# Optimization experiments

Hardware: AMD Instinct MI355X
Metric: run time of the kernel (lower is better)

Reference implementation:

```python
import jax, jax.numpy as jnp
import numpy as np

B, S, C = 32, 1024, 12      # sentences, words per sentence, chars per word
E, H = 256, 512             # embedding dim, word-LSTM hidden dim
V, CS, T = 50000, 128, 50   # vocab, charset, tagset


def _lstm(x, Wih, Whh, b):
    """Standard torch LSTM (gate order i,f,g,o). x: [T, N, I] -> hidden trace [T, N, H]."""
    Hd = Whh.shape[1]
    N = x.shape[1]
    h0 = jnp.zeros((N, Hd), x.dtype)
    c0 = jnp.zeros((N, Hd), x.dtype)

    def step(carry, xt):
        h, c = carry
        gates = xt @ Wih.T + h @ Whh.T + b
        i, f, g, o = jnp.split(gates, 4, axis=-1)
        c = jax.nn.sigmoid(f) * c + jax.nn.sigmoid(i) * jnp.tanh(g)
        h = jax.nn.sigmoid(o) * jnp.tanh(c)
        return (h, c), h

    _, hs = jax.lax.scan(step, (h0, c0), x)
    return hs


def setup_inputs() -> dict:
    key = jax.random.key(0)
    ks = jax.random.split(key, 12)
    sc = 0.05
    return {
        "char_idx": jax.random.randint(ks[0], (B, S, C), 0, CS),
        "word_idx": jax.random.randint(ks[1], (B, S), 0, V),
        "char_emb": jax.random.normal(ks[2], (CS, E), jnp.float32) * sc,
        "word_emb": jax.random.normal(ks[3], (V, E), jnp.float32) * sc,
        "Wc_ih": jax.random.normal(ks[4], (4 * E, E), jnp.float32) * sc,
        "Wc_hh": jax.random.normal(ks[5], (4 * E, E), jnp.float32) * sc,
        "bc": jnp.zeros((4 * E,), jnp.float32),
        "Ww_ih": jax.random.normal(ks[6], (4 * H, 2 * E), jnp.float32) * sc,
        "Ww_hh": jax.random.normal(ks[7], (4 * H, H), jnp.float32) * sc,
        "bw": jnp.zeros((4 * H,), jnp.float32),
        "Wt": jax.random.normal(ks[8], (T, H), jnp.float32) * sc,
        "bt": jnp.zeros((T,), jnp.float32),
    }


def reference(char_idx, word_idx, char_emb, word_emb, Wc_ih, Wc_hh, bc,
              Ww_ih, Ww_hh, bw, Wt, bt):
    # --- character-level LSTM: each word starts from a fresh zero state ---
    ce = char_emb[char_idx]                       # [B, S, C, E]
    ce = ce.reshape(B * S, C, E).transpose(1, 0, 2)  # [C, B*S, E]
    char_hs = _lstm(ce, Wc_ih, Wc_hh, bc)         # [C, B*S, E]
    char_feat = char_hs[-1].reshape(B, S, E)      # last char output per word

    # --- word-level LSTM over concatenated [word_emb ; char_feat] ---
    we = word_emb[word_idx]                       # [B, S, E]
    x = jnp.concatenate([we, char_feat], axis=-1) # [B, S, 2E]
    x = x.transpose(1, 0, 2)                      # [S, B, 2E]
    word_hs = _lstm(x, Ww_ih, Ww_hh, bw)          # [S, B, H]
    word_hs = word_hs.transpose(1, 0, 2)          # [B, S, H]

    # --- tag projection + log_softmax per token ---
    logits = word_hs @ Wt.T + bt                  # [B, S, T]
    return jax.nn.log_softmax(logits, axis=-1)
```

## Files before the change

kernel.cpp:

```cpp
#include <hip/hip_runtime.h>
#include <stdint.h>
#include <stddef.h>

#define NB   32
#define NS   1024
#define NC   12
#define NE   256
#define NH   512
#define NT   50
#define NWRD 32768
#define MC   1024
#define RW   2048
#define KW   512

typedef short bf16x8 __attribute__((ext_vector_type(8)));
typedef short bf16x4 __attribute__((ext_vector_type(4)));
typedef float f32x4  __attribute__((ext_vector_type(4)));
typedef unsigned int u32x4 __attribute__((ext_vector_type(4)));

#define MFMA16(a,b,c) __builtin_amdgcn_mfma_f32_16x16x32_bf16(a, b, c, 0, 0, 0)

__device__ __forceinline__ float bf2f(short u){
  return __uint_as_float(((uint32_t)(uint16_t)u) << 16);
}
__device__ __forceinline__ short f2bf(float f){
  uint32_t u = __float_as_uint(f);
  uint32_t r = (u + 0x7FFFu + ((u >> 16) & 1u)) >> 16;
  return (short)r;
}
__device__ __forceinline__ float sigf(float x){
  float e = __expf(-fabsf(x));
  float s = 1.0f / (1.0f + e);
  return x >= 0.0f ? s : 1.0f - s;
}
__device__ __forceinline__ float tanh_f(float x){
  float e = __expf(-2.0f * fabsf(x));
  float r = (1.0f - e) / (1.0f + e);
  return x >= 0.0f ? r : -r;
}

__global__ __launch_bounds__(256) void k_prep_pe(
    const float* __restrict__ char_emb, const float* __restrict__ Wc_ih,
    const float* __restrict__ bc, float* __restrict__ PEb)
{
  __shared__ float ce[NE];
  int a = blockIdx.x, tid = threadIdx.x;
  ce[tid] = char_emb[a * NE + tid];
  __syncthreads();
  int j = tid;
  float acc[4];
  #pragma unroll
  for (int g = 0; g < 4; ++g) acc[g] = 0.0f;
  for (int k = 0; k < NE; ++k) {
    float c = ce[k];
    #pragma unroll
    for (int g = 0; g < 4; ++g)
      acc[g] += c * Wc_ih[(size_t)(g * NE + j) * NE + k];
  }
  float4 o;
  o.x = acc[0] + bc[0 * NE + j];
  o.y = acc[1] + bc[1 * NE + j];
  o.z = acc[2] + bc[2 * NE + j];
  o.w = acc[3] + bc[3 * NE + j];
  *(float4*)&PEb[(size_t)a * MC + j * 4] = o;
}

__global__ __launch_bounds__(256) void k_prep_w(
    const float* __restrict__ Wc_hh, const float* __restrict__ Ww_ih,
    const float* __restrict__ Ww_hh, const float* __restrict__ bw,
    short* __restrict__ WhhC, short* __restrict__ WihW,
    short* __restrict__ WhhW, float* __restrict__ bwI)
{
  int r = blockIdx.x;
  int j = r >> 2, g = r & 3, tid = threadIdx.x;
  if (r < MC) {
    float v = Wc_hh[(size_t)(g * NE + j) * NE + tid];
    WhhC[(size_t)r * NE + tid] = f2bf(v);
  }
  #pragma unroll
  for (int kk = 0; kk < 2; ++kk) {
    int k = tid + kk * 256;
    WihW[(size_t)r * KW + k] = f2bf(Ww_ih[(size_t)(g * NH + j) * KW + k]);
    WhhW[(size_t)r * NH + k] = f2bf(Ww_hh[(size_t)(g * NH + j) * NH + k]);
  }
  if (tid == 0) bwI[r] = bw[g * NH + j];
}

__global__ __launch_bounds__(256) void k_char0(
    const int* __restrict__ char_idx, const float* __restrict__ PEb,
    float* __restrict__ c_state, short* __restrict__ h_out)
{
  int w = blockIdx.x, j = threadIdx.x;
  int idx = char_idx[w * NC + 0];
  float4 pe = *(const float4*)&PEb[(size_t)idx * MC + j * 4];
  float c = sigf(pe.x) * tanh_f(pe.z);
  float h = sigf(pe.w) * tanh_f(c);
  c_state[(size_t)w * NE + j] = c;
  h_out[(size_t)w * NE + j] = f2bf(h);
}

template<int KDIM, int EPI>
__global__ __launch_bounds__(256) void gemm_epi(
    const short* __restrict__ Amat, const short* __restrict__ Bmat,
    const float* __restrict__ PEb, const int* __restrict__ char_idx, int tstep,
    float* __restrict__ c_state, short* __restrict__ h_out,
    const float* __restrict__ bias, short* __restrict__ pw_out)
{
  __shared__ __align__(16) short As[128 * 64];
  __shared__ __align__(16) short Bs[128 * 64];
  const int tid = threadIdx.x;
  const int lane = tid & 63;
  const int wid = tid >> 6;
  const int wm = wid >> 1, wn = wid & 1;
  const int m0 = blockIdx.y * 128;
  const int n0 = blockIdx.x * 128;
  const int lo = lane & 15, hi = lane >> 4;

  f32x4 acc[4][4];
  #pragma unroll
  for (int i = 0; i < 4; ++i)
    #pragma unroll
    for (int j = 0; j < 4; ++j) acc[i][j] = (f32x4)0.0f;

  const int nk = KDIM / 64;
  for (int ki = 0; ki < nk; ++ki) {
    __syncthreads();
    #pragma unroll
    for (int it = 0; it < 4; ++it) {
      int cid = tid + it * 256;
      int row = cid >> 3, cp = cid & 7;
      int kch = cp ^ (row & 7);
      *(bf16x8*)&As[row * 64 + cp * 8] =
          *(const bf16x8*)&Amat[(size_t)(m0 + row) * KDIM + ki * 64 + kch * 8];
      *(bf16x8*)&Bs[row * 64 + cp * 8] =
          *(const bf16x8*)&Bmat[(size_t)(n0 + row) * KDIM + ki * 64 + kch * 8];
    }
    __syncthreads();
    #pragma unroll
    for (int kc = 0; kc < 2; ++kc) {
      bf16x8 af[4], bfr[4];
      #pragma unroll
      for (int fm = 0; fm < 4; ++fm) {
        int row = wm * 64 + fm * 16 + lo;
        int ch = (kc * 4 + hi) ^ (row & 7);
        af[fm] = *(bf16x8*)&As[row * 64 + ch * 8];
      }
      #pragma unroll
      for (int fn = 0; fn < 4; ++fn) {
        int row = wn * 64 + fn * 16 + lo;
        int ch = (kc * 4 + hi) ^ (row & 7);
        bfr[fn] = *(bf16x8*)&Bs[row * 64 + ch * 8];
      }
      #pragma unroll
      for (int fm = 0; fm < 4; ++fm)
        #pragma unroll
        for (int fn = 0; fn < 4; ++fn)
          acc[fm][fn] = MFMA16(af[fm], bfr[fn], acc[fm][fn]);
    }
  }

  #pragma unroll
  for (int fm = 0; fm < 4; ++fm) {
    int r0 = m0 + wm * 64 + fm * 16 + hi * 4;
    #pragma unroll
    for (int fn = 0; fn < 4; ++fn) {
      int w = n0 + wn * 64 + fn * 16 + lo;
      if constexpr (EPI == 0) {
        int idx = char_idx[w * NC + tstep];
        float4 pe = *(const float4*)&PEb[(size_t)idx * MC + r0];
        float gi = acc[fm][fn][0] + pe.x;
        float gf = acc[fm][fn][1] + pe.y;
        float gg = acc[fm][fn][2] + pe.z;
        float go = acc[fm][fn][3] + pe.w;
        int j = r0 >> 2;
        float c = sigf(gf) * c_state[(size_t)w * NE + j] + sigf(gi) * tanh_f(gg);
        c_state[(size_t)w * NE + j] = c;
        h_out[(size_t)w * NE + j] = f2bf(sigf(go) * tanh_f(c));
      } else {
        float4 bb = *(const float4*)&bias[r0];
        bf16x4 o;
        o[0] = f2bf(acc[fm][fn][0] + bb.x);
        o[1] = f2bf(acc[fm][fn][1] + bb.y);
        o[2] = f2bf(acc[fm][fn][2] + bb.z);
        o[3] = f2bf(acc[fm][fn][3] + bb.w);
        *(bf16x4*)&pw_out[(size_t)w * RW + r0] = o;
      }
    }
  }
}

__global__ __launch_bounds__(64) void k_xw(
    const int* __restrict__ word_idx, const float* __restrict__ word_emb,
    const short* __restrict__ h_char, short* __restrict__ Xw)
{
  int wp = blockIdx.x;
  int s = wp >> 5, b = wp & 31;
  int w = b * NS + s;
  int tid = threadIdx.x;
  int widx = word_idx[w];
  #pragma unroll
  for (int g = 0; g < 2; ++g) {
    int k4 = (tid + g * 64) * 4;
    bf16x4 o;
    if (k4 < NE) {
      float4 v = *(const float4*)&word_emb[(size_t)widx * NE + k4];
      o[0] = f2bf(v.x); o[1] = f2bf(v.y); o[2] = f2bf(v.z); o[3] = f2bf(v.w);
    } else {
      o = *(const bf16x4*)&h_char[(size_t)w * NE + (k4 - NE)];
    }
    *(bf16x4*)&Xw[(size_t)wp * KW + k4] = o;
  }
}

__global__ __launch_bounds__(512, 2) void k_word(
    const short* __restrict__ Whh,
    const short* __restrict__ PW,
    uint8_t* __restrict__ xb,
    short* __restrict__ word_hs)
{
  __shared__ __align__(16) short h_lds[2][32 * 520];
  const int tid = threadIdx.x, lane = tid & 63, wv = tid >> 6;
  const int lo = lane & 15, hi = lane >> 4;
  const int bk = blockIdx.x;
  const int wr = wv >> 1, wc = wv & 1;
  const int rowbase = bk * 64 + wr * 16;
  const int b = wc * 16 + lo;
  const int jl = (rowbase >> 2) + hi;
  const int r4 = rowbase + hi * 4;

  bf16x8 a[16];
  #pragma unroll
  for (int kc = 0; kc < 16; ++kc)
    a[kc] = *(const bf16x8*)&Whh[(size_t)(rowbase + lo) * NH + kc * 32 + hi * 8];

  short*    hdat  = (short*)xb;
  uint32_t* flags = (uint32_t*)(xb + 65536);

  const int db = tid >> 4, dlo = (tid & 15) * 8;
  const short* dA = hdat + db * 512 + dlo;
  const short* dB = dA + 16384;
  const uint32_t* fA = flags + lane * 4;
  const uint32_t* fB = fA + 256;

  float cst = 0.0f;
  bf16x4 pw = *(const bf16x4*)&PW[(size_t)b * RW + r4];

  for (int s = 0; s < NS; ++s) {
    const uint32_t tv = (uint32_t)s;
    const int par = s & 1;

    int sn = (s + 1 < NS) ? (s + 1) : (NS - 1);
    bf16x4 pwn = *(const bf16x4*)&PW[(size_t)(sn * NB + b) * RW + r4];

    {
      const uint32_t* fp = par ? fB : fA;
      int tries = 0;
      for (;;) {
        u32x4 f;
        asm volatile("global_load_dwordx4 %0, %1, off sc1\n\t"
                     "s_waitcnt vmcnt(0)"
                     : "=v"(f) : "v"(fp));
        bool ok = (f[0] == tv) & (f[1] == tv) & (f[2] == tv) & (f[3] == tv);
        if (__ballot(ok) == ~0ull) break;
        if (++tries > 768) {
          uint32_t g0 = __hip_atomic_load(fp + 0, __ATOMIC_RELAXED, __HIP_MEMORY_SCOPE_AGENT);
          uint32_t g1 = __hip_atomic_load(fp + 1, __ATOMIC_RELAXED, __HIP_MEMORY_SCOPE_AGENT);
          uint32_t g2 = __hip_atomic_load(fp + 2, __ATOMIC_RELAXED, __HIP_MEMORY_SCOPE_AGENT);
          uint32_t g3 = __hip_atomic_load(fp + 3, __ATOMIC_RELAXED, __HIP_MEMORY_SCOPE_AGENT);
          bool ok2 = (g0 == tv) & (g1 == tv) & (g2 == tv) & (g3 == tv);
          if (__ballot(ok2) == ~0ull) break;
          tries = 0;
        }
        __builtin_amdgcn_s_sleep(1);
      }
    }

    const short* sp = par ? dB : dA;
    bf16x8 d0, d1, d2, d3;
    asm volatile("global_load_dwordx4 %0, %4, off sc1\n\t"
                 "global_load_dwordx4 %1, %4, off offset:256 sc1\n\t"
                 "global_load_dwordx4 %2, %4, off offset:512 sc1\n\t"
                 "global_load_dwordx4 %3, %4, off offset:768 sc1\n\t"
                 "s_waitcnt vmcnt(0)"
                 : "=v"(d0), "=v"(d1), "=v"(d2), "=v"(d3) : "v"(sp));

    short* buf = &h_lds[par][0];
    short* dst = buf + db * 520 + dlo;
    *(bf16x8*)&dst[0]   = d0;
    *(bf16x8*)&dst[128] = d1;
    *(bf16x8*)&dst[256] = d2;
    *(bf16x8*)&dst[384] = d3;
    __syncthreads();

    f32x4 acc0, acc1, acc2, acc3;
    #pragma unroll
    for (int q = 0; q < 4; ++q) {
      acc0[q] = bf2f(pw[q]); acc1[q] = 0.0f; acc2[q] = 0.0f; acc3[q] = 0.0f;
    }
    #pragma unroll
    for (int kc = 0; kc < 16; kc += 4) {
      bf16x8 h0 = *(bf16x8*)((const char*)buf + b * 1040 + (kc + 0) * 64 + hi * 16);
      bf16x8 h1 = *(bf16x8*)((const char*)buf + b * 1040 + (kc + 1) * 64 + hi * 16);
      bf16x8 h2 = *(bf16x8*)((const char*)buf + b * 1040 + (kc + 2) * 64 + hi * 16);
      bf16x8 h3 = *(bf16x8*)((const char*)buf + b * 1040 + (kc + 3) * 64 + hi * 16);
      acc0 = MFMA16(a[kc + 0], h0, acc0);
      acc1 = MFMA16(a[kc + 1], h1, acc1);
      acc2 = MFMA16(a[kc + 2], h2, acc2);
      acc3 = MFMA16(a[kc + 3], h3, acc3);
    }
    f32x4 acc;
    #pragma unroll
    for (int q = 0; q < 4; ++q) acc[q] = (acc0[q] + acc1[q]) + (acc2[q] + acc3[q]);

    float c = sigf(acc[1]) * cst + sigf(acc[0]) * tanh_f(acc[2]);
    cst = c;
    short hv = f2bf(sigf(acc[3]) * tanh_f(c));

    unsigned int own = (unsigned int)(unsigned short)hv;
    unsigned int part = (unsigned int)__shfl_xor((int)own, 16);
    const int npar = (s + 1) & 1;
    if ((hi & 1) == 0) {
      unsigned int val = own | (part << 16);
      short* hp = hdat + (npar << 14) + b * 512 + jl;
      asm volatile("global_store_dword %0, %1, off sc1" :: "v"(hp), "v"(val) : "memory");
    }
    asm volatile("s_waitcnt vmcnt(0)" ::: "memory");
    if (lane == 0) {
      uint32_t* fq = flags + npar * 256 + bk * 8 + wv;
      asm volatile("global_store_dword %0, %1, off sc1"
                   :: "v"(fq), "v"((uint32_t)(s + 1)) : "memory");
    }
    word_hs[((size_t)b * NS + s) * NH + jl] = hv;
    pw = pwn;
  }
}

__global__ __launch_bounds__(256) void k_tags(
    const short* __restrict__ word_hs, const float* __restrict__ Wt,
    const float* __restrict__ bt, float* __restrict__ out)
{
  __shared__ __align__(16) short Ws[64 * 256];
  const int tid = threadIdx.x, lane = tid & 63, wid = tid >> 6;
  const int lo = lane & 15, hi = lane >> 4;
  const int n0 = blockIdx.x * 128;
  const int wb = n0 + wid * 32;

  f32x4 acc[4][2];
  #pragma unroll
  for (int fm = 0; fm < 4; ++fm)
    #pragma unroll
    for (int fn = 0; fn < 2; ++fn) acc[fm][fn] = (f32x4)0.0f;

  for (int half = 0; half < 2; ++half) {
    __syncthreads();
    for (int cid = tid; cid < 2048; cid += 256) {
      int row = cid >> 5, cp = cid & 31;
      int kch = cp ^ (row & 7);
      bf16x8 v;
      if (row < NT) {
        const float* src = &Wt[(size_t)row * KW + half * 256 + kch * 8];
        #pragma unroll
        for (int e = 0; e < 8; ++e) v[e] = f2bf(src[e]);
      } else v = (bf16x8)0;
      *(bf16x8*)&Ws[row * 256 + cp * 8] = v;
    }
    __syncthreads();
    #pragma unroll
    for (int kc = 0; kc < 8; ++kc) {
      bf16x8 bfr[2];
      #pragma unroll
      for (int fn = 0; fn < 2; ++fn) {
        int w = wb + fn * 16 + lo;
        bfr[fn] = *(const bf16x8*)&word_hs[(size_t)w * KW + half * 256 + kc * 32 + hi * 8];
      }
      #pragma unroll
      for (int fm = 0; fm < 4; ++fm) {
        int row = fm * 16 + lo;
        int ch = (kc * 4 + hi) ^ (row & 7);
        bf16x8 av = *(bf16x8*)&Ws[row * 256 + ch * 8];
        acc[fm][0] = MFMA16(av, bfr[0], acc[fm][0]);
        acc[fm][1] = MFMA16(av, bfr[1], acc[fm][1]);
      }
    }
  }

  #pragma unroll
  for (int fn = 0; fn < 2; ++fn) {
    int w = wb + fn * 16 + lo;
    float lg[16];
    float m = -1e30f;
    #pragma unroll
    for (int fm = 0; fm < 4; ++fm)
      #pragma unroll
      for (int q = 0; q < 4; ++q) {
        int tg = fm * 16 + hi * 4 + q;
        float bv = (tg < NT) ? bt[tg] : 0.0f;
        float v = acc[fm][fn][q] + bv;
        lg[fm * 4 + q] = v;
        if (tg < NT) m = fmaxf(m, v);
      }
    m = fmaxf(m, __shfl_xor(m, 16));
    m = fmaxf(m, __shfl_xor(m, 32));
    float s = 0.0f;
    #pragma unroll
    for (int fm = 0; fm < 4; ++fm)
      #pragma unroll
      for (int q = 0; q < 4; ++q) {
        int tg = fm * 16 + hi * 4 + q;
        if (tg < NT) s += __expf(lg[fm * 4 + q] - m);
      }
    s += __shfl_xor(s, 16);
    s += __shfl_xor(s, 32);
    float lz = m + __logf(s);
    #pragma unroll
    for (int fm = 0; fm < 4; ++fm)
      #pragma unroll
      for (int q = 0; q < 4; ++q) {
        int tg = fm * 16 + hi * 4 + q;
        if (tg < NT) out[(size_t)w * NT + tg] = lg[fm * 4 + q] - lz;
      }
  }
}

extern "C" void kernel_launch(void* const* d_in, const int* in_sizes, int n_in,
                              void* d_out, int out_size, void* d_ws, size_t ws_size,
                              hipStream_t stream) {
  const int*   char_idx = (const int*)  d_in[0];
  const int*   word_idx = (const int*)  d_in[1];
  const float* char_emb = (const float*)d_in[2];
  const float* word_emb = (const float*)d_in[3];
  const float* Wc_ih    = (const float*)d_in[4];
  const float* Wc_hh    = (const float*)d_in[5];
  const float* bc       = (const float*)d_in[6];
  const float* Ww_ih    = (const float*)d_in[7];
  const float* Ww_hh    = (const float*)d_in[8];
  const float* bw       = (const float*)d_in[9];
  const float* Wt       = (const float*)d_in[10];
  const float* bt       = (const float*)d_in[11];
  float* out = (float*)d_out;

  const size_t MB = 1ull << 20;
  uint8_t* w8 = (uint8_t*)d_ws;
  float* PEb   = (float*)(w8 + 0);
  short* WhhC  = (short*)(w8 + 512 * 1024);
  short* WihW  = (short*)(w8 + 1 * MB);
  short* WhhW  = (short*)(w8 + 3 * MB);
  float* bwI   = (float*)(w8 + 5 * MB);
  uint8_t* xb  = (uint8_t*)(w8 + 5 * MB + 64 * 1024);
  short* hA    = (short*)(w8 + 6 * MB);
  short* hB    = (short*)(w8 + 22 * MB);
  short* whs   = (short*)(w8 + 6 * MB);
  float* cC    = (float*)(w8 + 38 * MB);
  short* Xw    = (short*)(w8 + 38 * MB);
  short* PW    = (short*)(w8 + 70 * MB);

  k_prep_pe<<<128, 256, 0, stream>>>(char_emb, Wc_ih, bc, PEb);
  k_prep_w<<<2048, 256, 0, stream>>>(Wc_hh, Ww_ih, Ww_hh, bw, WhhC, WihW, WhhW, bwI);

  k_char0<<<NWRD, 256, 0, stream>>>(char_idx, PEb, cC, hA);
  for (int t = 1; t < NC; ++t) {
    short* src = (t & 1) ? hA : hB;
    short* dst = (t & 1) ? hB : hA;
    gemm_epi<256, 0><<<dim3(256, 8), 256, 0, stream>>>(
        WhhC, src, PEb, char_idx, t, cC, dst, nullptr, nullptr);
  }

  k_xw<<<NWRD, 64, 0, stream>>>(word_idx, word_emb, hB, Xw);
  gemm_epi<512, 1><<<dim3(256, 16), 256, 0, stream>>>(
      WihW, Xw, nullptr, nullptr, 0, nullptr, nullptr, bwI, PW);

  hipMemsetAsync(xb, 0, 64 * 1024 + 2048, stream);
  k_word<<<32, 512, 0, stream>>>(WhhW, PW, xb, whs);

  k_tags<<<256, 256, 0, stream>>>(whs, Wt, bt, out);
}
```

Measured before the change: 4.423 ms.

## Co-locate word-LSTM blocks on one XCD to use L2-coherent flag sync

Launches 256 blocks for the word LSTM, and each block reads its XCC id and takes a slot there. The first XCC to gather 32 blocks wins, and all other blocks exit. A runtime probe then checks whether sc0 stores and loads are visible across the 32 blocks. If they are, the recurrent loop uses sc0 (L2-local) accesses for the h exchange and step flags instead of sc1, cutting the cost of each per-step cross-block handshake. The PW prefetch is also deepened to two steps ahead. This adds launch overhead, relies on how blocks are scheduled and on hardware coherence behaviour, and falls back to the old sc1 path if the probe fails.

```diff
diff --git a/kernel.cpp b/kernel.cpp
--- a/kernel.cpp
+++ b/kernel.cpp
@@ -37,6 +37,12 @@
   float e = __expf(-2.0f * fabsf(x));
   float r = (1.0f - e) / (1.0f + e);
   return x >= 0.0f ? r : -r;
+}
+__device__ __forceinline__ uint32_t agent_ld(const uint32_t* p){
+  return __hip_atomic_load(p, __ATOMIC_RELAXED, __HIP_MEMORY_SCOPE_AGENT);
+}
+__device__ __forceinline__ void agent_st(uint32_t* p, uint32_t v){
+  __hip_atomic_store(p, v, __ATOMIC_RELAXED, __HIP_MEMORY_SCOPE_AGENT);
 }
 
 __global__ __launch_bounds__(256) void k_prep_pe(
@@ -212,16 +218,14 @@
   }
 }
 
-__global__ __launch_bounds__(512, 2) void k_word(
-    const short* __restrict__ Whh,
-    const short* __restrict__ PW,
-    uint8_t* __restrict__ xb,
-    short* __restrict__ word_hs)
-{
-  __shared__ __align__(16) short h_lds[2][32 * 520];
-  const int tid = threadIdx.x, lane = tid & 63, wv = tid >> 6;
+template<bool FAST>
+__device__ __forceinline__ void word_loop(
+    const short* __restrict__ Whh, const short* __restrict__ PW,
+    short* hdat, uint32_t* flags, short* __restrict__ word_hs,
+    short* h_lds, int bk, int tid)
+{
+  const int lane = tid & 63, wv = tid >> 6;
   const int lo = lane & 15, hi = lane >> 4;
-  const int bk = blockIdx.x;
   const int wr = wv >> 1, wc = wv & 1;
   const int rowbase = bk * 64 + wr * 16;
   const int b = wc * 16 + lo;
@@ -233,9 +237,6 @@
   for (int kc = 0; kc < 16; ++kc)
     a[kc] = *(const bf16x8*)&Whh[(size_t)(rowbase + lo) * NH + kc * 32 + hi * 8];
 
-  short*    hdat  = (short*)xb;
-  uint32_t* flags = (uint32_t*)(xb + 65536);
-
   const int db = tid >> 4, dlo = (tid & 15) * 8;
   const short* dA = hdat + db * 512 + dlo;
   const short* dB = dA + 16384;
@@ -243,33 +244,34 @@
   const uint32_t* fB = fA + 256;
 
   float cst = 0.0f;
-  bf16x4 pw = *(const bf16x4*)&PW[(size_t)b * RW + r4];
+  bf16x4 pw  = *(const bf16x4*)&PW[(size_t)(0 * NB + b) * RW + r4];
+  bf16x4 pw1 = *(const bf16x4*)&PW[(size_t)(1 * NB + b) * RW + r4];
 
   for (int s = 0; s < NS; ++s) {
     const uint32_t tv = (uint32_t)s;
     const int par = s & 1;
-
-    int sn = (s + 1 < NS) ? (s + 1) : (NS - 1);
-    bf16x4 pwn = *(const bf16x4*)&PW[(size_t)(sn * NB + b) * RW + r4];
 
     {
       const uint32_t* fp = par ? fB : fA;
       int tries = 0;
       for (;;) {
         u32x4 f;
-        asm volatile("global_load_dwordx4 %0, %1, off sc1\n\t"
-                     "s_waitcnt vmcnt(0)"
-                     : "=v"(f) : "v"(fp));
+        if constexpr (FAST)
+          asm volatile("global_load_dwordx4 %0, %1, off sc0\n\t"
+                       "s_waitcnt vmcnt(0)" : "=&v"(f) : "v"(fp));
+        else
+          asm volatile("global_load_dwordx4 %0, %1, off sc1\n\t"
+                       "s_waitcnt vmcnt(0)" : "=&v"(f) : "v"(fp));
         bool ok = (f[0] == tv) & (f[1] == tv) & (f[2] == tv) & (f[3] == tv);
         if (__ballot(ok) == ~0ull) break;
-        if (++tries > 768) {
-          uint32_t g0 = __hip_atomic_load(fp + 0, __ATOMIC_RELAXED, __HIP_MEMORY_SCOPE_AGENT);
-          uint32_t g1 = __hip_atomic_load(fp + 1, __ATOMIC_RELAXED, __HIP_MEMORY_SCOPE_AGENT);
-          uint32_t g2 = __hip_atomic_load(fp + 2, __ATOMIC_RELAXED, __HIP_MEMORY_SCOPE_AGENT);
-          uint32_t g3 = __hip_atomic_load(fp + 3, __ATOMIC_RELAXED, __HIP_MEMORY_SCOPE_AGENT);
-          bool ok2 = (g0 == tv) & (g1 == tv) & (g2 == tv) & (g3 == tv);
-          if (__ballot(ok2) == ~0ull) break;
-          tries = 0;
+        if constexpr (!FAST) {
+          if (++tries > 768) {
+            uint32_t g0 = agent_ld(fp + 0), g1 = agent_ld(fp + 1);
+            uint32_t g2 = agent_ld(fp + 2), g3 = agent_ld(fp + 3);
+            bool ok2 = (g0 == tv) & (g1 == tv) & (g2 == tv) & (g3 == tv);
+            if (__ballot(ok2) == ~0ull) break;
+            tries = 0;
+          }
         }
         __builtin_amdgcn_s_sleep(1);
       }
@@ -277,14 +279,22 @@
 
     const short* sp = par ? dB : dA;
     bf16x8 d0, d1, d2, d3;
-    asm volatile("global_load_dwordx4 %0, %4, off sc1\n\t"
-                 "global_load_dwordx4 %1, %4, off offset:256 sc1\n\t"
-                 "global_load_dwordx4 %2, %4, off offset:512 sc1\n\t"
-                 "global_load_dwordx4 %3, %4, off offset:768 sc1\n\t"
-                 "s_waitcnt vmcnt(0)"
-                 : "=v"(d0), "=v"(d1), "=v"(d2), "=v"(d3) : "v"(sp));
-
-    short* buf = &h_lds[par][0];
+    if constexpr (FAST)
+      asm volatile("global_load_dwordx4 %0, %4, off sc0\n\t"
+                   "global_load_dwordx4 %1, %4, off offset:256 sc0\n\t"
+                   "global_load_dwordx4 %2, %4, off offset:512 sc0\n\t"
+                   "global_load_dwordx4 %3, %4, off offset:768 sc0\n\t"
+                   "s_waitcnt vmcnt(0)"
+                   : "=&v"(d0), "=&v"(d1), "=&v"(d2), "=&v"(d3) : "v"(sp));
+    else
+      asm volatile("global_load_dwordx4 %0, %4, off sc1\n\t"
+                   "global_load_dwordx4 %1, %4, off offset:256 sc1\n\t"
+                   "global_load_dwordx4 %2, %4, off offset:512 sc1\n\t"
+                   "global_load_dwordx4 %3, %4, off offset:768 sc1\n\t"
+                   "s_waitcnt vmcnt(0)"
+                   : "=&v"(d0), "=&v"(d1), "=&v"(d2), "=&v"(d3) : "v"(sp));
+
+    short* buf = h_lds + par * (32 * 520);
     short* dst = buf + db * 520 + dlo;
     *(bf16x8*)&dst[0]   = d0;
     *(bf16x8*)&dst[128] = d1;
@@ -322,17 +332,118 @@
     if ((hi & 1) == 0) {
       unsigned int val = own | (part << 16);
       short* hp = hdat + (npar << 14) + b * 512 + jl;
-      asm volatile("global_store_dword %0, %1, off sc1" :: "v"(hp), "v"(val) : "memory");
+      if constexpr (FAST)
+        asm volatile("global_store_dword %0, %1, off sc0" :: "v"(hp), "v"(val) : "memory");
+      else
+        asm volatile("global_store_dword %0, %1, off sc1" :: "v"(hp), "v"(val) : "memory");
     }
     asm volatile("s_waitcnt vmcnt(0)" ::: "memory");
     if (lane == 0) {
       uint32_t* fq = flags + npar * 256 + bk * 8 + wv;
-      asm volatile("global_store_dword %0, %1, off sc1"
-                   :: "v"(fq), "v"((uint32_t)(s + 1)) : "memory");
+      if constexpr (FAST)
+        asm volatile("global_store_dword %0, %1, off sc0"
+                     :: "v"(fq), "v"((uint32_t)(s + 1)) : "memory");
+      else
+        asm volatile("global_store_dword %0, %1, off sc1"
+                     :: "v"(fq), "v"((uint32_t)(s + 1)) : "memory");
     }
     word_hs[((size_t)b * NS + s) * NH + jl] = hv;
-    pw = pwn;
-  }
+
+    int s2 = (s + 2 < NS) ? (s + 2) : (NS - 1);
+    bf16x4 pw2 = *(const bf16x4*)&PW[(size_t)(s2 * NB + b) * RW + r4];
+    pw = pw1; pw1 = pw2;
+  }
+}
+
+__global__ __launch_bounds__(512, 2) void k_word(
+    const short* __restrict__ Whh,
+    const short* __restrict__ PW,
+    uint8_t* __restrict__ xb,
+    short* __restrict__ word_hs)
+{
+  __shared__ __align__(16) short h_lds[2 * 32 * 520];
+  __shared__ int sh_bk, sh_fast;
+  const int tid = threadIdx.x;
+
+  short*    hdat  = (short*)xb;
+  uint32_t* flags = (uint32_t*)(xb + 65536);
+  uint32_t* cnt   = (uint32_t*)(xb + 67584);
+  uint32_t* win   = (uint32_t*)(xb + 67616);
+  uint32_t* probe = (uint32_t*)(xb + 67648);
+  uint32_t* rdy1  = (uint32_t*)(xb + 67776);
+  uint32_t* ack1  = (uint32_t*)(xb + 67904);
+  uint32_t* rdy2  = (uint32_t*)(xb + 68032);
+  uint32_t* verd  = (uint32_t*)(xb + 68160);
+
+  if (tid == 0) {
+    uint32_t xcc;
+    asm volatile("s_getreg_b32 %0, hwreg(HW_REG_XCC_ID)" : "=s"(xcc));
+    xcc &= 7u;
+    uint32_t slot = __hip_atomic_fetch_add(&cnt[xcc], 1u, __ATOMIC_RELAXED,
+                                           __HIP_MEMORY_SCOPE_AGENT);
+    if (slot == 31u) {
+      uint32_t exp = 0u;
+      __hip_atomic_compare_exchange_strong(win, &exp, xcc + 1u, __ATOMIC_RELAXED,
+                                           __ATOMIC_RELAXED, __HIP_MEMORY_SCOPE_AGENT);
+    }
+    uint32_t w;
+    for (;;) {
+      w = agent_ld(win);
+      if (w != 0u) break;
+      __builtin_amdgcn_s_sleep(8);
+    }
+    sh_bk = (w == xcc + 1u && slot < 32u) ? (int)slot : -1;
+  }
+  __syncthreads();
+  const int bk = sh_bk;
+  if (bk < 0) return;
+
+  if (tid == 0) {
+    if (bk == 0) {
+      asm volatile("global_store_dword %0, %1, off sc0" :: "v"(probe), "v"(0x11111111u) : "memory");
+      asm volatile("s_waitcnt vmcnt(0)" ::: "memory");
+      agent_st(rdy1, 1u);
+      uint32_t a;
+      for (;;) { a = agent_ld(ack1); if (a != 0u) break; __builtin_amdgcn_s_sleep(4); }
+      if (a == 1u) {
+        asm volatile("global_store_dword %0, %1, off sc0" :: "v"(probe), "v"(0x22222222u) : "memory");
+        asm volatile("s_waitcnt vmcnt(0)" ::: "memory");
+        agent_st(rdy2, 1u);
+      }
+    } else if (bk == 31) {
+      for (;;) { if (agent_ld(rdy1) != 0u) break; __builtin_amdgcn_s_sleep(4); }
+      bool okA = false;
+      for (int i = 0; i < 192 && !okA; ++i) {
+        uint32_t pv;
+        asm volatile("global_load_dword %0, %1, off sc0\n\ts_waitcnt vmcnt(0)"
+                     : "=&v"(pv) : "v"(probe));
+        okA = (pv == 0x11111111u);
+        if (!okA) __builtin_amdgcn_s_sleep(2);
+      }
+      agent_st(ack1, okA ? 1u : 2u);
+      bool okB = false;
+      if (okA) {
+        for (;;) { if (agent_ld(rdy2) != 0u) break; __builtin_amdgcn_s_sleep(4); }
+        for (int i = 0; i < 192 && !okB; ++i) {
+          uint32_t pv;
+          asm volatile("global_load_dword %0, %1, off sc0\n\ts_waitcnt vmcnt(0)"
+                       : "=&v"(pv) : "v"(probe));
+          okB = (pv == 0x22222222u);
+          if (!okB) __builtin_amdgcn_s_sleep(2);
+        }
+      }
+      agent_st(verd, okB ? 1u : 2u);
+    }
+    uint32_t v;
+    for (;;) { v = agent_ld(verd); if (v != 0u) break; __builtin_amdgcn_s_sleep(4); }
+    sh_fast = (v == 1u);
+  }
+  __syncthreads();
+
+  if (sh_fast)
+    word_loop<true >(Whh, PW, hdat, flags, word_hs, h_lds, bk, tid);
+  else
+    word_loop<false>(Whh, PW, hdat, flags, word_hs, h_lds, bk, tid);
 }
 
 __global__ __launch_bounds__(256) void k_tags(
@@ -469,8 +580,8 @@
   gemm_epi<512, 1><<<dim3(256, 16), 256, 0, stream>>>(
       WihW, Xw, nullptr, nullptr, 0, nullptr, nullptr, bwI, PW);
 
-  hipMemsetAsync(xb, 0, 64 * 1024 + 2048, stream);
-  k_word<<<32, 512, 0, stream>>>(WhhW, PW, xb, whs);
+  hipMemsetAsync(xb, 0, 69632, stream);
+  k_word<<<256, 512, 0, stream>>>(WhhW, PW, xb, whs);
 
   k_tags<<<256, 256, 0, stream>>>(whs, Wt, bt, out);
 }
```

Measured after the change: 4.499 ms. About the same (+1.7%).
